# Kernel optimization log

Hardware: AMD Instinct MI355X
Metric: run time of the kernel (lower is better)

The kernel has to match this reference:

```python
import jax, jax.numpy as jnp
import numpy as np

B, N, E, H, EF = 4, 10000, 160000, 128, 32

def dense(x, w, b):
    # Dense = Linear + SiLU activation
    return jax.nn.silu(x @ w + b)

def residual(x, w, b):
    # Residual(mlp_num=2): x + Dense(Dense(x))
    return x + dense(dense(x, w[0], b[0]), w[1], b[1])

def setup_inputs() -> dict:
    key = jax.random.key(0)
    ks = jax.random.split(key, 8)
    s = 0.05
    return dict(
        scalar=jax.random.normal(ks[0], (B, N, H), jnp.float32),
        ef=jax.random.normal(ks[1], (B, E, EF), jnp.float32),
        edge_index=jax.random.randint(ks[2], (B, E, 2), 0, N),
        C=jax.random.uniform(ks[3], (B, 1, 1), jnp.float32),
        emb_w=jax.random.normal(ks[4], (2, 2, H, H), jnp.float32) * s,
        emb_b=jnp.zeros((2, 2, H), jnp.float32),
        e_w=jax.random.normal(ks[5], (EF, H), jnp.float32) * s,
        conv_w=jax.random.normal(ks[6], (2, 2, H, H), jnp.float32) * s,
        conv_b=jnp.zeros((2, 2, H), jnp.float32),
        out_w=jax.random.normal(ks[7], (2, H, H), jnp.float32) * s,
        out_b=jnp.zeros((2, H), jnp.float32),
    )

def reference(scalar, ef, edge_index, C, emb_w, emb_b, e_w, conv_w, conv_b, out_w, out_b):
    row = edge_index[..., 0]   # [B,E] destination (scatter) indices
    col = edge_index[..., 1]   # [B,E] source (gather) indices
    # two 2-layer Dense MLPs on node features
    s2s = dense(dense(scalar, emb_w[0, 0], emb_b[0, 0]), emb_w[0, 1], emb_b[0, 1])       # [B,N,H]
    scalar_dst = dense(dense(scalar, emb_w[1, 0], emb_b[1, 0]), emb_w[1, 1], emb_b[1, 1])  # [B,N,H]
    ef_proj = ef @ e_w                                                                   # [B,E,H]
    # gather node feats at col, multiply by edge projection
    scalar_edge = jnp.take_along_axis(scalar_dst, col[..., None], axis=1) * ef_proj      # [B,E,H]
    # scatter-sum by row per batch element
    conv = jax.vmap(lambda x, r: jax.ops.segment_sum(x, r, num_segments=N))(scalar_edge, row)  # [B,N,H]
    conv = conv * C
    conv = residual(conv, conv_w[0], conv_b[0])
    conv = residual(conv, conv_w[1], conv_b[1])
    out = residual(s2s * conv, out_w, out_b)
    return out
```

## Files before the change

### kernel.cpp

```cpp
#include <hip/hip_runtime.h>
#include <hip/hip_bf16.h>

#define H 128
#define CAP 48
#define CSTRIDE 16

typedef _Float16 f16x4 __attribute__((ext_vector_type(4)));
typedef _Float16 f16x8 __attribute__((ext_vector_type(8)));
typedef float    f32x4 __attribute__((ext_vector_type(4)));

__device__ __forceinline__ float silu_f(float v) {
    return v / (1.0f + __expf(-v));
}

__global__ __launch_bounds__(256)
void pack_w(const float* __restrict__ emb_w, const float* __restrict__ conv_w,
            const float* __restrict__ out_w, const float* __restrict__ e_w,
            _Float16* __restrict__ wpk, int* __restrict__ cnt)
{
    const int gid = blockIdx.x * 256 + threadIdx.x;

#pragma unroll
    for (int i = 0; i < 32; ++i) {
        const int idx = gid + i * 20992;
        if (idx < 40960 * CSTRIDE) cnt[idx] = 0;
    }

    _Float16* dst = wpk + (size_t)gid * 8;
    if (gid < 20480) {
        const int mat = gid >> 11;
        const int r   = gid & 2047;
        const int ct  = r >> 8;
        const int kb  = (r >> 6) & 3;
        const int lane = r & 63;
        const float* W = (mat < 4) ? emb_w + mat * 16384
                       : (mat < 8) ? conv_w + (mat - 4) * 16384
                                   : out_w + (mat - 8) * 16384;
        const int m  = ct * 16 + (lane & 15);
        const int k0 = kb * 32 + (lane >> 4) * 8;
#pragma unroll
        for (int j = 0; j < 8; ++j)
            dst[j] = (_Float16)W[(k0 + j) * H + m];
    } else {
        const int r    = gid - 20480;
        const int ct   = r >> 6;
        const int lane = r & 63;
        const int m    = ct * 16 + (lane & 15);
        const int k0   = (lane >> 4) * 8;
#pragma unroll
        for (int j = 0; j < 8; ++j)
            dst[j] = (_Float16)e_w[(k0 + j) * H + m];
    }
}

template <int CT>
__device__ __forceinline__ void mfma_layerT(const _Float16* __restrict__ w,
                                            const f16x8 bf[4], int ct0, int lane,
                                            f32x4 acc[CT])
{
#pragma unroll
    for (int c = 0; c < CT; ++c) acc[c] = (f32x4){0.f, 0.f, 0.f, 0.f};
#pragma unroll
    for (int kb = 0; kb < 4; ++kb) {
#pragma unroll
        for (int ctl = 0; ctl < CT; ++ctl) {
            f16x8 af = *(const f16x8*)(w + ((size_t)((ct0 + ctl) * 4 + kb) * 64 + lane) * 8);
            acc[ctl] = __builtin_amdgcn_mfma_f32_16x16x32_f16(af, bf[kb], acc[ctl], 0, 0, 0);
        }
    }
}

template <int CT>
__device__ __forceinline__ void store_stripT(_Float16* strip, const f32x4 acc[CT],
                                             const float* bias, int ct0, int rl, int quad)
{
#pragma unroll
    for (int ctl = 0; ctl < CT; ++ctl) {
        const int c = (ct0 + ctl) * 16 + quad * 4;
        float4 bb = *(const float4*)(bias + c);
        f16x4 hv = {(_Float16)silu_f(acc[ctl][0] + bb.x),
                    (_Float16)silu_f(acc[ctl][1] + bb.y),
                    (_Float16)silu_f(acc[ctl][2] + bb.z),
                    (_Float16)silu_f(acc[ctl][3] + bb.w)};
        *(f16x4*)(strip + rl * 136 + c) = hv;
    }
}

template <int CT>
__device__ __forceinline__ void store_strip_rawT(_Float16* strip, const f32x4 t[CT],
                                                 int ct0, int rl, int quad)
{
#pragma unroll
    for (int ctl = 0; ctl < CT; ++ctl) {
        const int c = (ct0 + ctl) * 16 + quad * 4;
        f16x4 hv = {(_Float16)t[ctl][0], (_Float16)t[ctl][1],
                    (_Float16)t[ctl][2], (_Float16)t[ctl][3]};
        *(f16x4*)(strip + rl * 136 + c) = hv;
    }
}

__device__ __forceinline__ void load_bf(const _Float16* strip, f16x8 bf[4],
                                        int rl, int quad)
{
#pragma unroll
    for (int kb = 0; kb < 4; ++kb)
        bf[kb] = *(const f16x8*)(strip + rl * 136 + kb * 32 + quad * 8);
}

__global__ __launch_bounds__(256)
void embscat_k(const float* __restrict__ x, const _Float16* __restrict__ wpk,
               const float* __restrict__ emb_b,
               float* __restrict__ s2s, float* __restrict__ sdst,
               const int* __restrict__ eidx, int* __restrict__ cnt,
               unsigned* __restrict__ bucket, const float* __restrict__ ef)
{
    __shared__ _Float16 hs[4][16 * 136];
    const int g = blockIdx.x / 3, r = blockIdx.x % 3;

    if (r < 2) {
        const int e = (g * 2 + r) * 256 + threadIdx.x;
        const int2 rc = ((const int2*)eidx)[e];
        const int b = (unsigned)e / 160000u;
        const int key = b * 10000 + rc.x;
        const int pos = atomicAdd(&cnt[key * CSTRIDE], 1);
        if (pos < CAP)
            bucket[(size_t)key * CAP + pos] =
                ((unsigned)(e - b * 160000) << 14) | (unsigned)rc.y;
        const float w0 = ef[(size_t)e * 32];
        const float w1 = ef[(size_t)e * 32 + 16];
        asm volatile("" :: "v"(w0), "v"(w1));
        return;
    }

    const int tid  = threadIdx.x;
    const int lane = tid & 63;
    const int wid  = tid >> 6;
    const int msel = wid & 1;
    const int rg   = wid >> 1;
    const int rl   = lane & 15;
    const int quad = lane >> 4;
    const int row  = g * 32 + rg * 16 + rl;
    const size_t rbase = (size_t)row * H;

    f16x8 bf[4];
#pragma unroll
    for (int kb = 0; kb < 4; ++kb) {
        const int kc = kb * 32 + quad * 8;
        float4 v0 = *(const float4*)(x + rbase + kc);
        float4 v1 = *(const float4*)(x + rbase + kc + 4);
        bf[kb] = (f16x8){(_Float16)v0.x, (_Float16)v0.y, (_Float16)v0.z, (_Float16)v0.w,
                         (_Float16)v1.x, (_Float16)v1.y, (_Float16)v1.z, (_Float16)v1.w};
    }

    const _Float16* wm = wpk + (size_t)msel * 2 * 16384;
    _Float16* strip = hs[wid];
    const float* bias0 = emb_b + msel * 2 * H;

    f32x4 acc[8];
    mfma_layerT<8>(wm, bf, 0, lane, acc);
    store_stripT<8>(strip, acc, bias0, 0, rl, quad);
    __builtin_amdgcn_sched_barrier(0);
    load_bf(strip, bf, rl, quad);
    mfma_layerT<8>(wm + 16384, bf, 0, lane, acc);

    float* outp = msel ? sdst : s2s;
    const float* bias1 = bias0 + H;
#pragma unroll
    for (int ctl = 0; ctl < 8; ++ctl) {
        const int c = ctl * 16 + quad * 4;
        float4 bb = *(const float4*)(bias1 + c);
        float4 v;
        v.x = silu_f(acc[ctl][0] + bb.x);
        v.y = silu_f(acc[ctl][1] + bb.y);
        v.z = silu_f(acc[ctl][2] + bb.z);
        v.w = silu_f(acc[ctl][3] + bb.w);
        *(float4*)(outp + rbase + c) = v;
    }
}

__global__ __launch_bounds__(256)
void out6_k(const float* __restrict__ conv, const float* __restrict__ s2s,
            const _Float16* __restrict__ w6,
            const float* __restrict__ conv_b, const float* __restrict__ out_b,
            float* __restrict__ y)
{
    __shared__ _Float16 hs[4][16 * 136];
    const int tid  = threadIdx.x;
    const int lane = tid & 63;
    const int wid  = tid >> 6;
    const int rl   = lane & 15;
    const int quad = lane >> 4;
    const int row  = blockIdx.x * 64 + wid * 16 + rl;
    const size_t rbase = (size_t)row * H;
    _Float16* strip = hs[wid];

    f16x8 bf[4];
#pragma unroll
    for (int kb = 0; kb < 4; ++kb) {
        const int kc = kb * 32 + quad * 8;
        float4 v0 = *(const float4*)(conv + rbase + kc);
        float4 v1 = *(const float4*)(conv + rbase + kc + 4);
        bf[kb] = (f16x8){(_Float16)v0.x, (_Float16)v0.y, (_Float16)v0.z, (_Float16)v0.w,
                         (_Float16)v1.x, (_Float16)v1.y, (_Float16)v1.z, (_Float16)v1.w};
    }

    f32x4 acc[8], tD[8];

    mfma_layerT<8>(w6, bf, 0, lane, acc);
    store_stripT<8>(strip, acc, conv_b, 0, rl, quad);
    __builtin_amdgcn_sched_barrier(0);
    load_bf(strip, bf, rl, quad);

    mfma_layerT<8>(w6 + 16384, bf, 0, lane, acc);
#pragma unroll
    for (int ctl = 0; ctl < 8; ++ctl) {
        const int c = ctl * 16 + quad * 4;
        float4 bb = *(const float4*)(conv_b + H + c);
        float4 cv = *(const float4*)(conv + rbase + c);
        tD[ctl][0] = cv.x + silu_f(acc[ctl][0] + bb.x);
        tD[ctl][1] = cv.y + silu_f(acc[ctl][1] + bb.y);
        tD[ctl][2] = cv.z + silu_f(acc[ctl][2] + bb.z);
        tD[ctl][3] = cv.w + silu_f(acc[ctl][3] + bb.w);
    }
    store_strip_rawT<8>(strip, tD, 0, rl, quad);
    __builtin_amdgcn_sched_barrier(0);
    load_bf(strip, bf, rl, quad);

    mfma_layerT<8>(w6 + 2 * 16384, bf, 0, lane, acc);
    store_stripT<8>(strip, acc, conv_b + 2 * H, 0, rl, quad);
    __builtin_amdgcn_sched_barrier(0);
    load_bf(strip, bf, rl, quad);

    mfma_layerT<8>(w6 + 3 * 16384, bf, 0, lane, acc);
#pragma unroll
    for (int ctl = 0; ctl < 8; ++ctl) {
        const int c = ctl * 16 + quad * 4;
        float4 bb = *(const float4*)(conv_b + 3 * H + c);
        float4 sv = *(const float4*)(s2s + rbase + c);
        tD[ctl][0] = (tD[ctl][0] + silu_f(acc[ctl][0] + bb.x)) * sv.x;
        tD[ctl][1] = (tD[ctl][1] + silu_f(acc[ctl][1] + bb.y)) * sv.y;
        tD[ctl][2] = (tD[ctl][2] + silu_f(acc[ctl][2] + bb.z)) * sv.z;
        tD[ctl][3] = (tD[ctl][3] + silu_f(acc[ctl][3] + bb.w)) * sv.w;
    }
    store_strip_rawT<8>(strip, tD, 0, rl, quad);
    __builtin_amdgcn_sched_barrier(0);
    load_bf(strip, bf, rl, quad);

    mfma_layerT<8>(w6 + 4 * 16384, bf, 0, lane, acc);
    store_stripT<8>(strip, acc, out_b, 0, rl, quad);
    __builtin_amdgcn_sched_barrier(0);
    load_bf(strip, bf, rl, quad);

    mfma_layerT<8>(w6 + 5 * 16384, bf, 0, lane, acc);
#pragma unroll
    for (int ctl = 0; ctl < 8; ++ctl) {
        const int c = ctl * 16 + quad * 4;
        float4 bb = *(const float4*)(out_b + H + c);
        float4 v;
        v.x = tD[ctl][0] + silu_f(acc[ctl][0] + bb.x);
        v.y = tD[ctl][1] + silu_f(acc[ctl][1] + bb.y);
        v.z = tD[ctl][2] + silu_f(acc[ctl][2] + bb.z);
        v.w = tD[ctl][3] + silu_f(acc[ctl][3] + bb.w);
        *(float4*)(y + rbase + c) = v;
    }
}

#define GLD(dst, p, offlit) \
    asm volatile("global_load_dword %0, %1, off offset:" offlit \
                 : "=v"(dst) : "v"(p))
#define GLDX4(dst, p, offlit) \
    asm volatile("global_load_dwordx4 %0, %1, off offset:" offlit \
                 : "=v"(dst) : "v"(p))

__global__ __launch_bounds__(256, 2)
void conv_k(const float* __restrict__ ef, const float* __restrict__ sdst,
            const _Float16* __restrict__ ewpk, const float* __restrict__ C,
            const int* __restrict__ cnt, const unsigned* __restrict__ bucket,
            float* __restrict__ conv)
{
    const int tid  = threadIdx.x;
    const int lane = tid & 63;
    const int el   = lane & 15;
    const int quad = lane >> 4;
    const int nid  = blockIdx.x * 4 + (tid >> 6);
    const int b    = (unsigned)nid / 10000u;
    const int ebase = b * 160000;
    const int srow  = b * 10000;

    const int n = min(cnt[nid * CSTRIDE], CAP);
    const unsigned* bk = bucket + (size_t)nid * CAP;

    f16x8 bw[8];
#pragma unroll
    for (int ct = 0; ct < 8; ++ct)
        bw[ct] = *(const f16x8*)(ewpk + ((size_t)((ct << 6) + lane)) * 8);

    float part[8];
#pragma unroll
    for (int ct = 0; ct < 8; ++ct) part[ct] = 0.f;

#pragma unroll 1
    for (int base = 0; base < n; base += 16) {
        const int rem = n - base;
        const bool ok = (el < rem);
        const unsigned m = ok ? bk[base + el] : 0u;

        const int sc0 = srow + (__shfl((int)m, (quad << 2) | 0, 64) & 0x3FFF);
        const int sc1 = srow + (__shfl((int)m, (quad << 2) | 1, 64) & 0x3FFF);
        const int sc2 = srow + (__shfl((int)m, (quad << 2) | 2, 64) & 0x3FFF);
        const int sc3 = srow + (__shfl((int)m, (quad << 2) | 3, 64) & 0x3FFF);

        const float* pe = ef + (size_t)(ebase + (int)(m >> 14)) * 32 + (quad << 3);
        const float* p0 = sdst + (size_t)sc0 * H + el;
        const float* p1 = sdst + (size_t)sc1 * H + el;
        const float* p2 = sdst + (size_t)sc2 * H + el;
        const float* p3 = sdst + (size_t)sc3 * H + el;

        f32x4 v0, v1;
        GLDX4(v0, pe, "0");
        GLDX4(v1, pe, "16");
        float s0[8], s1[8], s2[8], s3[8];
        GLD(s0[0], p0, "0");   GLD(s0[1], p0, "64");  GLD(s0[2], p0, "128");
        GLD(s0[3], p0, "192"); GLD(s0[4], p0, "256"); GLD(s0[5], p0, "320");
        GLD(s0[6], p0, "384"); GLD(s0[7], p0, "448");
        GLD(s1[0], p1, "0");   GLD(s1[1], p1, "64");  GLD(s1[2], p1, "128");
        GLD(s1[3], p1, "192"); GLD(s1[4], p1, "256"); GLD(s1[5], p1, "320");
        GLD(s1[6], p1, "384"); GLD(s1[7], p1, "448");
        GLD(s2[0], p2, "0");   GLD(s2[1], p2, "64");  GLD(s2[2], p2, "128");
        GLD(s2[3], p2, "192"); GLD(s2[4], p2, "256"); GLD(s2[5], p2, "320");
        GLD(s2[6], p2, "384"); GLD(s2[7], p2, "448");
        GLD(s3[0], p3, "0");   GLD(s3[1], p3, "64");  GLD(s3[2], p3, "128");
        GLD(s3[3], p3, "192"); GLD(s3[4], p3, "256"); GLD(s3[5], p3, "320");
        GLD(s3[6], p3, "384"); GLD(s3[7], p3, "448");

        asm volatile("s_waitcnt vmcnt(0)" ::: "memory");
        __builtin_amdgcn_sched_barrier(0);

        const f16x8 af = {
            ok ? (_Float16)v0[0] : (_Float16)0.f, ok ? (_Float16)v0[1] : (_Float16)0.f,
            ok ? (_Float16)v0[2] : (_Float16)0.f, ok ? (_Float16)v0[3] : (_Float16)0.f,
            ok ? (_Float16)v1[0] : (_Float16)0.f, ok ? (_Float16)v1[1] : (_Float16)0.f,
            ok ? (_Float16)v1[2] : (_Float16)0.f, ok ? (_Float16)v1[3] : (_Float16)0.f};

#pragma unroll
        for (int ct = 0; ct < 8; ++ct) {
            f32x4 acc = __builtin_amdgcn_mfma_f32_16x16x32_f16(
                af, bw[ct], (f32x4){0.f, 0.f, 0.f, 0.f}, 0, 0, 0);
            part[ct] += acc[0] * s0[ct] + acc[1] * s1[ct]
                      + acc[2] * s2[ct] + acc[3] * s3[ct];
        }
    }

    const float Cb = C[b];
    float w0 = 0.f, w1 = 0.f;
#pragma unroll
    for (int ct = 0; ct < 8; ++ct) {
        float v = part[ct];
        v += __shfl_xor(v, 16, 64);
        v += __shfl_xor(v, 32, 64);
        v *= Cb;
        if ((ct >> 1) == quad) { if (ct & 1) w1 = v; else w0 = v; }
    }
    float* dst = conv + (size_t)nid * H + (quad << 5) + el;
    dst[0]  = w0;
    dst[16] = w1;
}

extern "C" void kernel_launch(void* const* d_in, const int* in_sizes, int n_in,
                              void* d_out, int out_size, void* d_ws, size_t ws_size,
                              hipStream_t stream)
{
    const float* scalar = (const float*)d_in[0];
    const float* ef     = (const float*)d_in[1];
    const int*   eidx   = (const int*)d_in[2];
    const float* C      = (const float*)d_in[3];
    const float* emb_w  = (const float*)d_in[4];
    const float* emb_b  = (const float*)d_in[5];
    const float* e_w    = (const float*)d_in[6];
    const float* conv_w = (const float*)d_in[7];
    const float* conv_b = (const float*)d_in[8];
    const float* out_w  = (const float*)d_in[9];
    const float* out_b  = (const float*)d_in[10];

    const int M = 40000;
    const size_t nodeElems = (size_t)M * H;

    float* s2s  = (float*)d_ws;
    float* sdst = s2s + nodeElems;
    float* conv = sdst + nodeElems;
    _Float16* wpk = (_Float16*)(conv + nodeElems);
    int* cnt    = (int*)(wpk + 167936);
    unsigned* bucket = (unsigned*)(cnt + 40960 * CSTRIDE);

    dim3 blk(256);

    pack_w<<<82, blk, 0, stream>>>(emb_w, conv_w, out_w, e_w, wpk, cnt);
    embscat_k<<<3750, blk, 0, stream>>>(scalar, wpk, emb_b, s2s, sdst,
                                        eidx, cnt, bucket, ef);
    conv_k<<<10000, blk, 0, stream>>>(ef, sdst, wpk + 163840, C, cnt, bucket, conv);
    out6_k<<<625, blk, 0, stream>>>(conv, s2s, wpk + 4 * 16384,
                                    conv_b, out_b, (float*)d_out);
}
```

Measured before the change: 303.1 us.

## Fuse edge-conv aggregation with output residual MLP chain into one kernel

```diff
diff --git a/kernel.cpp b/kernel.cpp
--- a/kernel.cpp
+++ b/kernel.cpp
@@ -178,63 +178,160 @@
     }
 }
 
-__global__ __launch_bounds__(256)
-void out6_k(const float* __restrict__ conv, const float* __restrict__ s2s,
-            const _Float16* __restrict__ w6,
-            const float* __restrict__ conv_b, const float* __restrict__ out_b,
-            float* __restrict__ y)
-{
-    __shared__ _Float16 hs[4][16 * 136];
+#define GLD(dst, p, offlit) \
+    asm volatile("global_load_dword %0, %1, off offset:" offlit \
+                 : "=v"(dst) : "v"(p))
+#define GLDX4(dst, p, offlit) \
+    asm volatile("global_load_dwordx4 %0, %1, off offset:" offlit \
+                 : "=v"(dst) : "v"(p))
+
+__global__ __launch_bounds__(256, 3)
+void convout_k(const float* __restrict__ ef, const float* __restrict__ sdst,
+               const _Float16* __restrict__ ewpk, const float* __restrict__ C,
+               const int* __restrict__ cnt, const unsigned* __restrict__ bucket,
+               const float* __restrict__ s2s, const _Float16* __restrict__ w6,
+               const float* __restrict__ conv_b, const float* __restrict__ out_b,
+               float* __restrict__ y)
+{
+    __shared__ _Float16 hsC[16 * 136];
+    __shared__ float    cvf[16 * 128];
+    __shared__ _Float16 hs0[16 * 136], hs1[16 * 136];
+
     const int tid  = threadIdx.x;
     const int lane = tid & 63;
+    const int el   = lane & 15;
+    const int quad = lane >> 4;
     const int wid  = tid >> 6;
-    const int rl   = lane & 15;
-    const int quad = lane >> 4;
-    const int row  = blockIdx.x * 64 + wid * 16 + rl;
+    const int nbase = blockIdx.x * 16;
+    const int b     = nbase / 10000;
+    const int ebase = b * 160000;
+    const int srow  = b * 10000;
+    const float Cb  = C[b];
+
+    f16x8 bw[8];
+#pragma unroll
+    for (int ct = 0; ct < 8; ++ct)
+        bw[ct] = *(const f16x8*)(ewpk + ((size_t)((ct << 6) + lane)) * 8);
+
+#pragma unroll 1
+    for (int j = 0; j < 4; ++j) {
+        const int nid = nbase + wid * 4 + j;
+        const int n = min(cnt[nid * CSTRIDE], CAP);
+        const unsigned* bk = bucket + (size_t)nid * CAP;
+
+        float part[8];
+#pragma unroll
+        for (int ct = 0; ct < 8; ++ct) part[ct] = 0.f;
+
+#pragma unroll 1
+        for (int base = 0; base < n; base += 16) {
+            const int rem = n - base;
+            const bool ok = (el < rem);
+            const unsigned m = ok ? bk[base + el] : 0u;
+
+            const int sc0 = srow + (__shfl((int)m, (quad << 2) | 0, 64) & 0x3FFF);
+            const int sc1 = srow + (__shfl((int)m, (quad << 2) | 1, 64) & 0x3FFF);
+            const int sc2 = srow + (__shfl((int)m, (quad << 2) | 2, 64) & 0x3FFF);
+            const int sc3 = srow + (__shfl((int)m, (quad << 2) | 3, 64) & 0x3FFF);
+
+            const float* pe = ef + (size_t)(ebase + (int)(m >> 14)) * 32 + (quad << 3);
+            const float* p0 = sdst + (size_t)sc0 * H + el;
+            const float* p1 = sdst + (size_t)sc1 * H + el;
+            const float* p2 = sdst + (size_t)sc2 * H + el;
+            const float* p3 = sdst + (size_t)sc3 * H + el;
+
+            f32x4 v0, v1;
+            GLDX4(v0, pe, "0");
+            GLDX4(v1, pe, "16");
+            float s0[8], s1[8], s2[8], s3[8];
+            GLD(s0[0], p0, "0");   GLD(s0[1], p0, "64");  GLD(s0[2], p0, "128");
+            GLD(s0[3], p0, "192"); GLD(s0[4], p0, "256"); GLD(s0[5], p0, "320");
+            GLD(s0[6], p0, "384"); GLD(s0[7], p0, "448");
+            GLD(s1[0], p1, "0");   GLD(s1[1], p1, "64");  GLD(s1[2], p1, "128");
+            GLD(s1[3], p1, "192"); GLD(s1[4], p1, "256"); GLD(s1[5], p1, "320");
+            GLD(s1[6], p1, "384"); GLD(s1[7], p1, "448");
+            GLD(s2[0], p2, "0");   GLD(s2[1], p2, "64");  GLD(s2[2], p2, "128");
+            GLD(s2[3], p2, "192"); GLD(s2[4], p2, "256"); GLD(s2[5], p2, "320");
+            GLD(s2[6], p2, "384"); GLD(s2[7], p2, "448");
+            GLD(s3[0], p3, "0");   GLD(s3[1], p3, "64");  GLD(s3[2], p3, "128");
+            GLD(s3[3], p3, "192"); GLD(s3[4], p3, "256"); GLD(s3[5], p3, "320");
+            GLD(s3[6], p3, "384"); GLD(s3[7], p3, "448");
+
+            asm volatile("s_waitcnt vmcnt(0)" ::: "memory");
+            __builtin_amdgcn_sched_barrier(0);
+
+            const f16x8 af = {
+                ok ? (_Float16)v0[0] : (_Float16)0.f, ok ? (_Float16)v0[1] : (_Float16)0.f,
+                ok ? (_Float16)v0[2] : (_Float16)0.f, ok ? (_Float16)v0[3] : (_Float16)0.f,
+                ok ? (_Float16)v1[0] : (_Float16)0.f, ok ? (_Float16)v1[1] : (_Float16)0.f,
+                ok ? (_Float16)v1[2] : (_Float16)0.f, ok ? (_Float16)v1[3] : (_Float16)0.f};
+
+#pragma unroll
+            for (int ct = 0; ct < 8; ++ct) {
+                f32x4 acc = __builtin_amdgcn_mfma_f32_16x16x32_f16(
+                    af, bw[ct], (f32x4){0.f, 0.f, 0.f, 0.f}, 0, 0, 0);
+                part[ct] += acc[0] * s0[ct] + acc[1] * s1[ct]
+                          + acc[2] * s2[ct] + acc[3] * s3[ct];
+            }
+        }
+
+        const int lr = wid * 4 + j;
+        float w0 = 0.f, w1 = 0.f;
+#pragma unroll
+        for (int ct = 0; ct < 8; ++ct) {
+            float v = part[ct];
+            v += __shfl_xor(v, 16, 64);
+            v += __shfl_xor(v, 32, 64);
+            v *= Cb;
+            if ((ct >> 1) == quad) { if (ct & 1) w1 = v; else w0 = v; }
+        }
+        const int c0 = (quad << 5) + el;
+        cvf[lr * 128 + c0]      = w0;
+        cvf[lr * 128 + c0 + 16] = w1;
+        hsC[lr * 136 + c0]      = (_Float16)w0;
+        hsC[lr * 136 + c0 + 16] = (_Float16)w1;
+    }
+    __syncthreads();
+
+    const int ct0 = wid * 2;
+    const int rl  = el;
+    const int row = nbase + rl;
     const size_t rbase = (size_t)row * H;
-    _Float16* strip = hs[wid];
 
     f16x8 bf[4];
-#pragma unroll
-    for (int kb = 0; kb < 4; ++kb) {
-        const int kc = kb * 32 + quad * 8;
-        float4 v0 = *(const float4*)(conv + rbase + kc);
-        float4 v1 = *(const float4*)(conv + rbase + kc + 4);
-        bf[kb] = (f16x8){(_Float16)v0.x, (_Float16)v0.y, (_Float16)v0.z, (_Float16)v0.w,
-                         (_Float16)v1.x, (_Float16)v1.y, (_Float16)v1.z, (_Float16)v1.w};
-    }
-
-    f32x4 acc[8], tD[8];
-
-    mfma_layerT<8>(w6, bf, 0, lane, acc);
-    store_stripT<8>(strip, acc, conv_b, 0, rl, quad);
-    __builtin_amdgcn_sched_barrier(0);
-    load_bf(strip, bf, rl, quad);
-
-    mfma_layerT<8>(w6 + 16384, bf, 0, lane, acc);
-#pragma unroll
-    for (int ctl = 0; ctl < 8; ++ctl) {
-        const int c = ctl * 16 + quad * 4;
+    load_bf(hsC, bf, rl, quad);
+
+    f32x4 acc[2], tD[2];
+
+    mfma_layerT<2>(w6, bf, ct0, lane, acc);
+    store_stripT<2>(hs0, acc, conv_b, ct0, rl, quad);
+    __syncthreads();
+    load_bf(hs0, bf, rl, quad);
+
+    mfma_layerT<2>(w6 + 16384, bf, ct0, lane, acc);
+#pragma unroll
+    for (int ctl = 0; ctl < 2; ++ctl) {
+        const int c = (ct0 + ctl) * 16 + quad * 4;
         float4 bb = *(const float4*)(conv_b + H + c);
-        float4 cv = *(const float4*)(conv + rbase + c);
+        float4 cv = *(const float4*)(cvf + rl * 128 + c);
         tD[ctl][0] = cv.x + silu_f(acc[ctl][0] + bb.x);
         tD[ctl][1] = cv.y + silu_f(acc[ctl][1] + bb.y);
         tD[ctl][2] = cv.z + silu_f(acc[ctl][2] + bb.z);
         tD[ctl][3] = cv.w + silu_f(acc[ctl][3] + bb.w);
     }
-    store_strip_rawT<8>(strip, tD, 0, rl, quad);
-    __builtin_amdgcn_sched_barrier(0);
-    load_bf(strip, bf, rl, quad);
-
-    mfma_layerT<8>(w6 + 2 * 16384, bf, 0, lane, acc);
-    store_stripT<8>(strip, acc, conv_b + 2 * H, 0, rl, quad);
-    __builtin_amdgcn_sched_barrier(0);
-    load_bf(strip, bf, rl, quad);
-
-    mfma_layerT<8>(w6 + 3 * 16384, bf, 0, lane, acc);
-#pragma unroll
-    for (int ctl = 0; ctl < 8; ++ctl) {
-        const int c = ctl * 16 + quad * 4;
+    store_strip_rawT<2>(hs1, tD, ct0, rl, quad);
+    __syncthreads();
+    load_bf(hs1, bf, rl, quad);
+
+    mfma_layerT<2>(w6 + 2 * 16384, bf, ct0, lane, acc);
+    store_stripT<2>(hs0, acc, conv_b + 2 * H, ct0, rl, quad);
+    __syncthreads();
+    load_bf(hs0, bf, rl, quad);
+
+    mfma_layerT<2>(w6 + 3 * 16384, bf, ct0, lane, acc);
+#pragma unroll
+    for (int ctl = 0; ctl < 2; ++ctl) {
+        const int c = (ct0 + ctl) * 16 + quad * 4;
         float4 bb = *(const float4*)(conv_b + 3 * H + c);
         float4 sv = *(const float4*)(s2s + rbase + c);
         tD[ctl][0] = (tD[ctl][0] + silu_f(acc[ctl][0] + bb.x)) * sv.x;
@@ -242,19 +339,19 @@
         tD[ctl][2] = (tD[ctl][2] + silu_f(acc[ctl][2] + bb.z)) * sv.z;
         tD[ctl][3] = (tD[ctl][3] + silu_f(acc[ctl][3] + bb.w)) * sv.w;
     }
-    store_strip_rawT<8>(strip, tD, 0, rl, quad);
-    __builtin_amdgcn_sched_barrier(0);
-    load_bf(strip, bf, rl, quad);
-
-    mfma_layerT<8>(w6 + 4 * 16384, bf, 0, lane, acc);
-    store_stripT<8>(strip, acc, out_b, 0, rl, quad);
-    __builtin_amdgcn_sched_barrier(0);
-    load_bf(strip, bf, rl, quad);
-
-    mfma_layerT<8>(w6 + 5 * 16384, bf, 0, lane, acc);
-#pragma unroll
-    for (int ctl = 0; ctl < 8; ++ctl) {
-        const int c = ctl * 16 + quad * 4;
+    store_strip_rawT<2>(hs1, tD, ct0, rl, quad);
+    __syncthreads();
+    load_bf(hs1, bf, rl, quad);
+
+    mfma_layerT<2>(w6 + 4 * 16384, bf, ct0, lane, acc);
+    store_stripT<2>(hs0, acc, out_b, ct0, rl, quad);
+    __syncthreads();
+    load_bf(hs0, bf, rl, quad);
+
+    mfma_layerT<2>(w6 + 5 * 16384, bf, ct0, lane, acc);
+#pragma unroll
+    for (int ctl = 0; ctl < 2; ++ctl) {
+        const int c = (ct0 + ctl) * 16 + quad * 4;
         float4 bb = *(const float4*)(out_b + H + c);
         float4 v;
         v.x = tD[ctl][0] + silu_f(acc[ctl][0] + bb.x);
@@ -263,107 +360,6 @@
         v.w = tD[ctl][3] + silu_f(acc[ctl][3] + bb.w);
         *(float4*)(y + rbase + c) = v;
     }
-}
-
-#define GLD(dst, p, offlit) \
-    asm volatile("global_load_dword %0, %1, off offset:" offlit \
-                 : "=v"(dst) : "v"(p))
-#define GLDX4(dst, p, offlit) \
-    asm volatile("global_load_dwordx4 %0, %1, off offset:" offlit \
-                 : "=v"(dst) : "v"(p))
-
-__global__ __launch_bounds__(256, 2)
-void conv_k(const float* __restrict__ ef, const float* __restrict__ sdst,
-            const _Float16* __restrict__ ewpk, const float* __restrict__ C,
-            const int* __restrict__ cnt, const unsigned* __restrict__ bucket,
-            float* __restrict__ conv)
-{
-    const int tid  = threadIdx.x;
-    const int lane = tid & 63;
-    const int el   = lane & 15;
-    const int quad = lane >> 4;
-    const int nid  = blockIdx.x * 4 + (tid >> 6);
-    const int b    = (unsigned)nid / 10000u;
-    const int ebase = b * 160000;
-    const int srow  = b * 10000;
-
-    const int n = min(cnt[nid * CSTRIDE], CAP);
-    const unsigned* bk = bucket + (size_t)nid * CAP;
-
-    f16x8 bw[8];
-#pragma unroll
-    for (int ct = 0; ct < 8; ++ct)
-        bw[ct] = *(const f16x8*)(ewpk + ((size_t)((ct << 6) + lane)) * 8);
-
-    float part[8];
-#pragma unroll
-    for (int ct = 0; ct < 8; ++ct) part[ct] = 0.f;
-
-#pragma unroll 1
-    for (int base = 0; base < n; base += 16) {
-        const int rem = n - base;
-        const bool ok = (el < rem);
-        const unsigned m = ok ? bk[base + el] : 0u;
-
-        const int sc0 = srow + (__shfl((int)m, (quad << 2) | 0, 64) & 0x3FFF);
-        const int sc1 = srow + (__shfl((int)m, (quad << 2) | 1, 64) & 0x3FFF);
-        const int sc2 = srow + (__shfl((int)m, (quad << 2) | 2, 64) & 0x3FFF);
-        const int sc3 = srow + (__shfl((int)m, (quad << 2) | 3, 64) & 0x3FFF);
-
-        const float* pe = ef + (size_t)(ebase + (int)(m >> 14)) * 32 + (quad << 3);
-        const float* p0 = sdst + (size_t)sc0 * H + el;
-        const float* p1 = sdst + (size_t)sc1 * H + el;
-        const float* p2 = sdst + (size_t)sc2 * H + el;
-        const float* p3 = sdst + (size_t)sc3 * H + el;
-
-        f32x4 v0, v1;
-        GLDX4(v0, pe, "0");
-        GLDX4(v1, pe, "16");
-        float s0[8], s1[8], s2[8], s3[8];
-        GLD(s0[0], p0, "0");   GLD(s0[1], p0, "64");  GLD(s0[2], p0, "128");
-        GLD(s0[3], p0, "192"); GLD(s0[4], p0, "256"); GLD(s0[5], p0, "320");
-        GLD(s0[6], p0, "384"); GLD(s0[7], p0, "448");
-        GLD(s1[0], p1, "0");   GLD(s1[1], p1, "64");  GLD(s1[2], p1, "128");
-        GLD(s1[3], p1, "192"); GLD(s1[4], p1, "256"); GLD(s1[5], p1, "320");
-        GLD(s1[6], p1, "384"); GLD(s1[7], p1, "448");
-        GLD(s2[0], p2, "0");   GLD(s2[1], p2, "64");  GLD(s2[2], p2, "128");
-        GLD(s2[3], p2, "192"); GLD(s2[4], p2, "256"); GLD(s2[5], p2, "320");
-        GLD(s2[6], p2, "384"); GLD(s2[7], p2, "448");
-        GLD(s3[0], p3, "0");   GLD(s3[1], p3, "64");  GLD(s3[2], p3, "128");
-        GLD(s3[3], p3, "192"); GLD(s3[4], p3, "256"); GLD(s3[5], p3, "320");
-        GLD(s3[6], p3, "384"); GLD(s3[7], p3, "448");
-
-        asm volatile("s_waitcnt vmcnt(0)" ::: "memory");
-        __builtin_amdgcn_sched_barrier(0);
-
-        const f16x8 af = {
-            ok ? (_Float16)v0[0] : (_Float16)0.f, ok ? (_Float16)v0[1] : (_Float16)0.f,
-            ok ? (_Float16)v0[2] : (_Float16)0.f, ok ? (_Float16)v0[3] : (_Float16)0.f,
-            ok ? (_Float16)v1[0] : (_Float16)0.f, ok ? (_Float16)v1[1] : (_Float16)0.f,
-            ok ? (_Float16)v1[2] : (_Float16)0.f, ok ? (_Float16)v1[3] : (_Float16)0.f};
-
-#pragma unroll
-        for (int ct = 0; ct < 8; ++ct) {
-            f32x4 acc = __builtin_amdgcn_mfma_f32_16x16x32_f16(
-                af, bw[ct], (f32x4){0.f, 0.f, 0.f, 0.f}, 0, 0, 0);
-            part[ct] += acc[0] * s0[ct] + acc[1] * s1[ct]
-                      + acc[2] * s2[ct] + acc[3] * s3[ct];
-        }
-    }
-
-    const float Cb = C[b];
-    float w0 = 0.f, w1 = 0.f;
-#pragma unroll
-    for (int ct = 0; ct < 8; ++ct) {
-        float v = part[ct];
-        v += __shfl_xor(v, 16, 64);
-        v += __shfl_xor(v, 32, 64);
-        v *= Cb;
-        if ((ct >> 1) == quad) { if (ct & 1) w1 = v; else w0 = v; }
-    }
-    float* dst = conv + (size_t)nid * H + (quad << 5) + el;
-    dst[0]  = w0;
-    dst[16] = w1;
 }
 
 extern "C" void kernel_launch(void* const* d_in, const int* in_sizes, int n_in,
@@ -387,8 +383,7 @@
 
     float* s2s  = (float*)d_ws;
     float* sdst = s2s + nodeElems;
-    float* conv = sdst + nodeElems;
-    _Float16* wpk = (_Float16*)(conv + nodeElems);
+    _Float16* wpk = (_Float16*)(sdst + nodeElems);
     int* cnt    = (int*)(wpk + 167936);
     unsigned* bucket = (unsigned*)(cnt + 40960 * CSTRIDE);
 
@@ -397,7 +392,7 @@
     pack_w<<<82, blk, 0, stream>>>(emb_w, conv_w, out_w, e_w, wpk, cnt);
     embscat_k<<<3750, blk, 0, stream>>>(scalar, wpk, emb_b, s2s, sdst,
                                         eidx, cnt, bucket, ef);
-    conv_k<<<10000, blk, 0, stream>>>(ef, sdst, wpk + 163840, C, cnt, bucket, conv);
-    out6_k<<<625, blk, 0, stream>>>(conv, s2s, wpk + 4 * 16384,
-                                    conv_b, out_b, (float*)d_out);
-}
+    convout_k<<<2500, blk, 0, stream>>>(ef, sdst, wpk + 163840, C, cnt, bucket,
+                                        s2s, wpk + 4 * 16384,
+                                        conv_b, out_b, (float*)d_out);
+}
```

After: 274.6 us. -9.4%, faster.
